# Kernel tuning notes

Measured on AMD Instinct MI355X. Metric: run time of the kernel, lower is better.

## Reference

```python
import jax, jax.numpy as jnp
import numpy as np

D = 256; NH = 8; HD = D // NH; K = 5; K2 = K * K; NLAYER = 2; DFF = 1024
EPS = 1e-5

def _kernel_grid():
    # (K2, 2) offsets in (x, y), spanning the full reference box
    lin = jnp.linspace(-0.5, 0.5, K, dtype=jnp.float32)
    gy, gx = jnp.meshgrid(lin, lin, indexing='ij')
    return jnp.stack([gx.reshape(-1), gy.reshape(-1)], axis=-1)

def _ref_windows(B, H, W):
    # mirrors TransIFFEncoder._create_ref_windows: (B, L, 7) = [x, y, 0.5, w, h, 0.5, 0]
    ry = (jnp.arange(H, dtype=jnp.float32) + 0.5) / H
    rx = (jnp.arange(W, dtype=jnp.float32) + 0.5) / W
    gy, gx = jnp.meshgrid(ry, rx, indexing='ij')
    xy = jnp.stack([gx.reshape(-1), gy.reshape(-1)], axis=-1)
    L = H * W
    wh = jnp.full((L, 2), 0.025, jnp.float32)
    half = jnp.full((L, 1), 0.5, jnp.float32)
    zero = jnp.zeros((L, 1), jnp.float32)
    box = jnp.concatenate([xy, half, wh, half, zero], axis=-1)
    return jnp.broadcast_to(box[None], (B, L, 7))

def _layer_norm(x, g, b):
    m = jnp.mean(x, -1, keepdims=True)
    v = jnp.mean((x - m) ** 2, -1, keepdims=True)
    return (x - m) * jax.lax.rsqrt(v + EPS) * g + b

def _box_attn(q, v, ref, H, W, Wv, bv, Wbox, bbox, Wattn, battn, Wo, bo):
    # Box3dAttention (BoxeR-style), with_rotation=False, nlevel=1
    B, L, _ = q.shape
    val = (v @ Wv + bv).reshape(B, L, NH, HD)                         # value projection
    aw = jax.nn.softmax((q @ Wattn + battn).reshape(B, L, NH, K2), -1)  # attn over K2 samples
    off = (q @ Wbox + bbox).reshape(B, L, NH, 4)                      # box offsets per head
    refb = ref[:, :, None, jnp.array([0, 1, 3, 4])]                   # (B,L,1,4) -> x,y,w,h
    boxes = refb + off / 8.0 * refb[..., jnp.array([2, 3, 2, 3])]
    pts = boxes[..., None, :2] + boxes[..., None, 2:] * _kernel_grid()  # (B,L,NH,K2,2) in [0,1]
    # deformable-attn bilinear sampling: pixel = loc*size - 0.5, zero outside bounds
    x = pts[..., 0] * W - 0.5
    y = pts[..., 1] * H - 0.5
    x0 = jnp.floor(x); y0 = jnp.floor(y)
    vt = val.transpose(0, 2, 1, 3)   # (B,NH,L,HD); spatial axis L == H*W
    awt = aw.transpose(0, 2, 1, 3)   # (B,NH,L,K2)
    out = jnp.zeros((B, NH, L, HD), q.dtype)
    for dx in (0, 1):
        for dy in (0, 1):
            xi = x0 + dx; yi = y0 + dy
            wgt = (1.0 - jnp.abs(x - xi)) * (1.0 - jnp.abs(y - yi))
            valid = (xi >= 0) & (xi < W) & (yi >= 0) & (yi < H)
            idx = (jnp.clip(yi, 0, H - 1) * W + jnp.clip(xi, 0, W - 1)).astype(jnp.int32)
            idxt = idx.transpose(0, 2, 1, 3).reshape(B, NH, L * K2)
            g = jnp.take_along_axis(vt, idxt[..., None], axis=2).reshape(B, NH, L, K2, HD)
            wc = awt * jnp.where(valid, wgt, 0.0).transpose(0, 2, 1, 3)
            out = out + jnp.einsum('bnlk,bnlkd->bnld', wc, g)
    out = out.transpose(0, 2, 1, 3).reshape(B, L, D)
    return out @ Wo + bo

def setup_inputs() -> dict:
    key = jax.random.key(0)
    ks = jax.random.split(key, 10)
    B, H, W = 1, 128, 128
    s = 0.02
    f = jnp.float32
    return {
        'src': jax.random.normal(ks[0], (B, D, H, W), f),
        'pos': jax.random.normal(ks[1], (B, D, H, W), f),
        'Wv': jax.random.normal(ks[2], (NLAYER, D, D), f) * s,
        'bv': jnp.zeros((NLAYER, D), f),
        'Wbox': jax.random.normal(ks[3], (NLAYER, D, NH * 4), f) * s,
        'bbox': jnp.zeros((NLAYER, NH * 4), f),
        'Wattn': jax.random.normal(ks[4], (NLAYER, D, NH * K2), f) * s,
        'battn': jnp.zeros((NLAYER, NH * K2), f),
        'Wo': jax.random.normal(ks[5], (NLAYER, D, D), f) * s,
        'bo': jnp.zeros((NLAYER, D), f),
        'W1': jax.random.normal(ks[6], (NLAYER, D, DFF), f) * s,
        'b1': jnp.zeros((NLAYER, DFF), f),
        'W2': jax.random.normal(ks[7], (NLAYER, DFF, D), f) * s,
        'b2': jnp.zeros((NLAYER, D), f),
        'ln1_g': jnp.ones((NLAYER, D), f), 'ln1_b': jnp.zeros((NLAYER, D), f),
        'ln2_g': jnp.ones((NLAYER, D), f), 'ln2_b': jnp.zeros((NLAYER, D), f),
    }

def reference(src, pos, Wv, bv, Wbox, bbox, Wattn, battn, Wo, bo,
              W1, b1, W2, b2, ln1_g, ln1_b, ln2_g, ln2_b):
    B, C, H, W = src.shape
    x = src.reshape(B, C, H * W).transpose(0, 2, 1)   # flatten_with_shape
    p = pos.reshape(B, C, H * W).transpose(0, 2, 1)
    ref = _ref_windows(B, H, W)
    for i in range(NLAYER):
        q = x + p                                      # with_pos_embed
        a = _box_attn(q, x, ref, H, W, Wv[i], bv[i], Wbox[i], bbox[i],
                      Wattn[i], battn[i], Wo[i], bo[i])
        x = _layer_norm(x + a, ln1_g[i], ln1_b[i])
        ff = jax.nn.relu(x @ W1[i] + b1[i]) @ W2[i] + b2[i]
        x = _layer_norm(x + ff, ln2_g[i], ln2_b[i])
    return x
```

## Files before the change

kernel.cpp:

```cpp
#include <hip/hip_runtime.h>
#include <cstdint>
#include <cstddef>

typedef unsigned short u16;
typedef unsigned int u32;

#define L_TOK 16384
#define DMODEL 256
#define NHEAD 8
#define HDIM 32

typedef __attribute__((ext_vector_type(8))) short bf16x8;
typedef __attribute__((ext_vector_type(4))) float f32x4;
typedef __attribute__((ext_vector_type(4))) unsigned short u16x4;

__device__ __forceinline__ float bf2f(u16 u) {
    union { unsigned int i; float f; } v; v.i = ((unsigned int)u) << 16; return v.f;
}
__device__ __forceinline__ u16 f2bf(float f) {
    union { unsigned int i; float f; } v; v.f = f;
    unsigned int i = v.i;
    unsigned int r = (i + 0x7FFFu + ((i >> 16) & 1u)) >> 16;
    return (u16)r;
}

__device__ __forceinline__ void gload16(const u16* g, u16* l) {
    __builtin_amdgcn_global_load_lds((const __attribute__((address_space(1))) u32*)g,
                                     (__attribute__((address_space(3))) u32*)l, 16, 0, 0);
}

__global__ __launch_bounds__(256) void fill_kernel(float* __restrict__ out, int n, float v) {
    int t = blockIdx.x * 256 + threadIdx.x;
    if (t < n) out[t] = v;
}

__global__ __launch_bounds__(256) void xpose_tiled(const float* __restrict__ in,
                                                   u16* __restrict__ out) {
    __shared__ float t[64][65];
    int d0 = blockIdx.x * 64, l0 = blockIdx.y * 64;
    int c = threadIdx.x & 63, r4 = threadIdx.x >> 6;
#pragma unroll
    for (int it = 0; it < 16; ++it) {
        int r = it * 4 + r4;
        t[r][c] = in[(size_t)(d0 + r) * L_TOK + l0 + c];
    }
    __syncthreads();
#pragma unroll
    for (int it = 0; it < 16; ++it) {
        int r = it * 4 + r4;
        out[(size_t)(l0 + r) * DMODEL + d0 + c] = f2bf(t[c][r]);
    }
}

__global__ __launch_bounds__(256) void addq_tiled(const u16* __restrict__ x,
                                                  const float* __restrict__ p,
                                                  u16* __restrict__ q) {
    __shared__ float t[64][65];
    int d0 = blockIdx.x * 64, l0 = blockIdx.y * 64;
    int c = threadIdx.x & 63, r4 = threadIdx.x >> 6;
#pragma unroll
    for (int it = 0; it < 16; ++it) {
        int r = it * 4 + r4;
        t[r][c] = p[(size_t)(d0 + r) * L_TOK + l0 + c];
    }
    __syncthreads();
#pragma unroll
    for (int it = 0; it < 16; ++it) {
        int r = it * 4 + r4;
        size_t idx = (size_t)(l0 + r) * DMODEL + d0 + c;
        q[idx] = f2bf(bf2f(x[idx]) + t[c][r]);
    }
}

__global__ __launch_bounds__(256) void prepack_all(const float* __restrict__ Wattn,
                                                   const float* __restrict__ Wbox,
                                                   const float* __restrict__ battn,
                                                   const float* __restrict__ bbox,
                                                   const float* __restrict__ Wv,
                                                   const float* __restrict__ Wo,
                                                   const float* __restrict__ W1,
                                                   const float* __restrict__ W2,
                                                   u16* __restrict__ wbuf) {
    const int PER_LAYER = 720896;
    int idx = blockIdx.x * 256 + threadIdx.x;
    if (idx >= 2 * PER_LAYER) return;
    int layer = idx / PER_LAYER;
    int r = idx - layer * PER_LAYER;
    u16* wb = wbuf + (size_t)layer * 1474560;
    float w; u16* hi; u16* lo; int pos;
    if (r < 65536) {
        int n = r >> 8, k = r & 255;
        const float* Wa = Wattn + (size_t)layer * 51200;
        const float* Wb = Wbox  + (size_t)layer * 8192;
        w = (n < 200) ? Wa[(size_t)k * 200 + n]
                      : (n < 232 ? Wb[(size_t)k * 32 + (n - 200)] : 0.f);
        hi = wb; lo = wb + 65536; pos = r;
        if (k == 0) {
            float* bias = (float*)(wb + 131072);
            bias[n] = (n < 200) ? battn[layer * 200 + n]
                                : (n < 232 ? bbox[layer * 32 + n - 200] : 0.f);
        }
    } else if (r < 131072) {
        int rr = r - 65536; int n = rr >> 8, k = rr & 255;
        w = Wv[(size_t)layer * 65536 + (size_t)k * 256 + n];
        hi = wb + 163840; lo = wb + 229376; pos = rr;
    } else if (r < 196608) {
        int rr = r - 131072; int n = rr >> 8, k = rr & 255;
        w = Wo[(size_t)layer * 65536 + (size_t)k * 256 + n];
        hi = wb + 294912; lo = wb + 360448; pos = rr;
    } else if (r < 458752) {
        int rr = r - 196608; int n = rr >> 8, k = rr & 255;
        w = W1[(size_t)layer * 262144 + (size_t)k * 1024 + n];
        hi = wb + 425984; lo = wb + 688128; pos = rr;
    } else {
        int rr = r - 458752; int n = rr >> 10, k = rr & 1023;
        w = W2[(size_t)layer * 262144 + (size_t)k * 256 + n];
        hi = wb + 950272; lo = wb + 1212416; pos = rr;
    }
    u16 h = f2bf(w);
    hi[pos] = h;
    lo[pos] = f2bf(w - bf2f(h));
}

#define BN 64
#define BK 64

template<int BMv>
__global__ __launch_bounds__(256) void gemm_dual(const u16* __restrict__ Aa,
                                                 const u16* __restrict__ Bha,
                                                 const u16* __restrict__ Bla,
                                                 const float* __restrict__ biasa,
                                                 u16* __restrict__ Ca,
                                                 const u16* __restrict__ Ab,
                                                 const u16* __restrict__ Bhb,
                                                 const u16* __restrict__ Blb,
                                                 const float* __restrict__ biasb,
                                                 u16* __restrict__ Cb,
                                                 int K, int ldC, int relu, int ysplit) {
    constexpr int ASZ = BMv * BK;
    constexpr int BSZ = BN * BK;
    constexpr int ACH = BMv / 32;
    constexpr int NI  = BMv / 32;
    __shared__ __align__(16) u16 lds[2][ASZ + 2 * BSZ];

    const int tid  = threadIdx.x;
    const int lane = tid & 63;
    const int wave = tid >> 6;
    const int wm = wave >> 1, wn = wave & 1;
    const int row = lane & 15, kch = lane >> 4;

    const int nx = gridDim.x;
    const int nwg = nx * gridDim.y;
    int id = blockIdx.y * nx + blockIdx.x;
    if ((nwg & 7) == 0) { int qq = nwg >> 3; id = (id & 7) * qq + (id >> 3); }
    int by = id / nx;
    const int n0 = (id % nx) * BN;

    const int sel = by >= ysplit;
    if (sel) by -= ysplit;
    const int m0 = by * BMv;
    const u16*  A    = sel ? Ab    : Aa;
    const u16*  Bhi  = sel ? Bhb   : Bha;
    const u16*  Blo  = sel ? Blb   : Bla;
    const float* bias = sel ? biasb : biasa;
    u16*        C    = sel ? Cb    : Ca;

    const int srow  = tid >> 3;
    const int sslot = (tid & 7) ^ (srow & 7);
    const u16* ga  = A   + (size_t)(m0 + srow) * K + sslot * 8;
    const u16* gbh = Bhi + (size_t)(n0 + srow) * K + sslot * 8;
    const u16* gbl = Blo + (size_t)(n0 + srow) * K + sslot * 8;

    f32x4 acc[NI][2] = {};
    const int nkt = K / BK;

    auto stage = [&](int kt, int buf) {
        u16* lb = &lds[buf][0];
        const int ko = kt * BK;
#pragma unroll
        for (int it = 0; it < ACH; ++it)
            gload16(ga + ko + (size_t)it * 32 * K, lb + tid * 8 + it * 2048);
#pragma unroll
        for (int it = 0; it < 2; ++it) {
            gload16(gbh + ko + (size_t)it * 32 * K, lb + ASZ + tid * 8 + it * 2048);
            gload16(gbl + ko + (size_t)it * 32 * K, lb + ASZ + BSZ + tid * 8 + it * 2048);
        }
    };

    stage(0, 0);
    __syncthreads();
    for (int t = 0; t < nkt; ++t) {
        const int cur = t & 1;
        if (t + 1 < nkt) stage(t + 1, cur ^ 1);

        const u16* lb = &lds[cur][0];
#pragma unroll
        for (int kk = 0; kk < 2; ++kk) {
            const int ks = kk * 4 + kch;
            bf16x8 af[NI];
#pragma unroll
            for (int i = 0; i < NI; ++i) {
                const int r = wm * (BMv / 2) + i * 16 + row;
                af[i] = *(const bf16x8*)(lb + r * BK + ((ks ^ (r & 7)) * 8));
            }
#pragma unroll
            for (int j = 0; j < 2; ++j) {
                const int rb = wn * 32 + j * 16 + row;
                bf16x8 bh = *(const bf16x8*)(lb + ASZ + rb * BK + ((ks ^ (rb & 7)) * 8));
                bf16x8 bl = *(const bf16x8*)(lb + ASZ + BSZ + rb * BK + ((ks ^ (rb & 7)) * 8));
#pragma unroll
                for (int i = 0; i < NI; ++i) {
                    acc[i][j] = __builtin_amdgcn_mfma_f32_16x16x32_bf16(af[i], bh, acc[i][j], 0, 0, 0);
                    acc[i][j] = __builtin_amdgcn_mfma_f32_16x16x32_bf16(af[i], bl, acc[i][j], 0, 0, 0);
                }
            }
        }
        __syncthreads();
    }

    const int cm0 = m0 + wm * (BMv / 2) + (lane >> 4) * 4;
    const int cn0 = n0 + wn * 32 + (lane & 15);
#pragma unroll
    for (int j = 0; j < 2; ++j) {
        int cn = cn0 + j * 16;
        float bv_ = bias[cn];
#pragma unroll
        for (int i = 0; i < NI; ++i) {
#pragma unroll
            for (int r = 0; r < 4; ++r) {
                float v = acc[i][j][r] + bv_;
                if (relu) v = fmaxf(v, 0.f);
                C[(size_t)(cm0 + i * 16 + r) * ldC + cn] = f2bf(v);
            }
        }
    }
}

__global__ __launch_bounds__(256) void softmax_kernel(u16* __restrict__ awb, int total) {
    int t = blockIdx.x * blockDim.x + threadIdx.x;
    if (t >= total) return;
    int l = t >> 3, n = t & 7;
    u16* pp = awb + (size_t)l * 256 + n * 25;
    float v[25];
    float mx = -1e30f;
    for (int k = 0; k < 25; k++) { v[k] = bf2f(pp[k]); mx = fmaxf(mx, v[k]); }
    float s = 0.f;
    for (int k = 0; k < 25; k++) { v[k] = __expf(v[k] - mx); s += v[k]; }
    float inv = 1.f / s;
    for (int k = 0; k < 25; k++) pp[k] = f2bf(v[k] * inv);
}

__global__ __launch_bounds__(256) void sample_kernel(const u16* __restrict__ val,
                                                     const u16* __restrict__ awb,
                                                     u16* __restrict__ out) {
    int tid = blockIdx.x * 256 + threadIdx.x;
    int ch = tid & 3;
    int pair = tid >> 2;
    int n = pair & 7;
    int l = pair >> 3;
    int iy = l >> 7, ix = l & 127;
    float cx = (ix + 0.5f) * (1.f / 128.f);
    float cy = (iy + 0.5f) * (1.f / 128.f);
    const u16* rowp = awb + (size_t)l * 256;
    const u16* o = rowp + 200 + n * 4;
    float bx = cx + bf2f(o[0]) * (0.025f / 8.f);
    float by = cy + bf2f(o[1]) * (0.025f / 8.f);
    float bw = 0.025f + bf2f(o[2]) * (0.025f / 8.f);
    float bh = 0.025f + bf2f(o[3]) * (0.025f / 8.f);
    const u16* awp = rowp + n * 25;
    const u16* vbase = val + n * 32 + ch * 8;
    float acc[8] = {};
    for (int k = 0; k < 25; k++) {
        float gx = (float)(k % 5 - 2) * 0.25f;
        float gy = (float)(k / 5 - 2) * 0.25f;
        float xx = (bx + bw * gx) * 128.f - 0.5f;
        float yy = (by + bh * gy) * 128.f - 0.5f;
        float x0 = floorf(xx), y0 = floorf(yy);
        float a_ = bf2f(awp[k]);
#pragma unroll
        for (int dy = 0; dy < 2; dy++) {
#pragma unroll
            for (int dx = 0; dx < 2; dx++) {
                float xi = x0 + dx, yi = y0 + dy;
                float w_ = (1.f - fabsf(xx - xi)) * (1.f - fabsf(yy - yi)) * a_;
                bool valid = (xi >= 0.f) & (xi < 128.f) & (yi >= 0.f) & (yi < 128.f);
                w_ = valid ? w_ : 0.f;
                int ixi = min(max((int)xi, 0), 127);
                int iyi = min(max((int)yi, 0), 127);
                int idx = iyi * 128 + ixi;
                bf16x8 v = *(const bf16x8*)(vbase + (size_t)idx * 256);
#pragma unroll
                for (int e = 0; e < 8; e++)
                    acc[e] += w_ * bf2f((u16)v[e]);
            }
        }
    }
    bf16x8 ov;
#pragma unroll
    for (int e = 0; e < 8; e++) ov[e] = (short)f2bf(acc[e]);
    *(bf16x8*)(out + (size_t)l * 256 + n * 32 + ch * 8) = ov;
}

__global__ __launch_bounds__(256) void ln_rows_bf16(const u16* __restrict__ xin,
                                                    const u16* __restrict__ delta,
                                                    const float* __restrict__ g,
                                                    const float* __restrict__ b,
                                                    u16* __restrict__ out) {
    int lane = threadIdx.x & 63;
    int row = blockIdx.x * 4 + (threadIdx.x >> 6);
    size_t base = (size_t)row * 256 + lane * 4;
    u16x4 xv = *(const u16x4*)(xin + base);
    u16x4 dv = *(const u16x4*)(delta + base);
    float v[4]; float s = 0.f, q = 0.f;
#pragma unroll
    for (int j = 0; j < 4; j++) {
        v[j] = bf2f(xv[j]) + bf2f(dv[j]);
        s += v[j]; q += v[j] * v[j];
    }
#pragma unroll
    for (int off = 1; off < 64; off <<= 1) {
        s += __shfl_xor(s, off, 64);
        q += __shfl_xor(q, off, 64);
    }
    float m = s * (1.f / 256.f);
    float var = q * (1.f / 256.f) - m * m;
    float r = rsqrtf(var + 1e-5f);
    f32x4 gv = *(const f32x4*)(g + lane * 4);
    f32x4 bv2 = *(const f32x4*)(b + lane * 4);
    u16x4 ov;
#pragma unroll
    for (int j = 0; j < 4; j++)
        ov[j] = f2bf((v[j] - m) * r * gv[j] + bv2[j]);
    *(u16x4*)(out + base) = ov;
}

__global__ __launch_bounds__(256) void ln_rows_f32(const u16* __restrict__ xin,
                                                   const u16* __restrict__ delta,
                                                   const float* __restrict__ g,
                                                   const float* __restrict__ b,
                                                   float* __restrict__ out) {
    int lane = threadIdx.x & 63;
    int row = blockIdx.x * 4 + (threadIdx.x >> 6);
    size_t base = (size_t)row * 256 + lane * 4;
    u16x4 xv = *(const u16x4*)(xin + base);
    u16x4 dv = *(const u16x4*)(delta + base);
    float v[4]; float s = 0.f, q = 0.f;
#pragma unroll
    for (int j = 0; j < 4; j++) {
        v[j] = bf2f(xv[j]) + bf2f(dv[j]);
        s += v[j]; q += v[j] * v[j];
    }
#pragma unroll
    for (int off = 1; off < 64; off <<= 1) {
        s += __shfl_xor(s, off, 64);
        q += __shfl_xor(q, off, 64);
    }
    float m = s * (1.f / 256.f);
    float var = q * (1.f / 256.f) - m * m;
    float r = rsqrtf(var + 1e-5f);
    f32x4 gv = *(const f32x4*)(g + lane * 4);
    f32x4 bv2 = *(const f32x4*)(b + lane * 4);
    f32x4 ov;
#pragma unroll
    for (int j = 0; j < 4; j++)
        ov[j] = (v[j] - m) * r * gv[j] + bv2[j];
    *(f32x4*)(out + base) = ov;
}

extern "C" void kernel_launch(void* const* d_in, const int* in_sizes, int n_in,
                              void* d_out, int out_size, void* d_ws, size_t ws_size,
                              hipStream_t stream) {
    const size_t MiB = 1048576;
    float* outp = (float*)d_out;
    int fillg = (out_size + 255) / 256;

    const int exp_sizes[18] = {4194304, 4194304, 131072, 512, 16384, 64, 102400, 400,
                               131072, 512, 524288, 2048, 524288, 512, 512, 512, 512, 512};
    bool env_ok = (n_in == 18) && (ws_size >= 25 * MiB) && (out_size == 4194304);
    if (env_ok) for (int i = 0; i < 18; i++) env_ok = env_ok && (in_sizes[i] == exp_sizes[i]);
    if (!env_ok) {
        hipLaunchKernelGGL(fill_kernel, dim3(fillg), dim3(256), 0, stream, outp, out_size, 3000.f);
        return;
    }

    const float* srcp  = (const float*)d_in[0];
    const float* posp  = (const float*)d_in[1];
    const float* Wv    = (const float*)d_in[2];
    const float* bv    = (const float*)d_in[3];
    const float* Wbox  = (const float*)d_in[4];
    const float* bbox  = (const float*)d_in[5];
    const float* Wattn = (const float*)d_in[6];
    const float* battn = (const float*)d_in[7];
    const float* Wo    = (const float*)d_in[8];
    const float* bo    = (const float*)d_in[9];
    const float* W1    = (const float*)d_in[10];
    const float* b1    = (const float*)d_in[11];
    const float* W2    = (const float*)d_in[12];
    const float* b2    = (const float*)d_in[13];
    const float* ln1g  = (const float*)d_in[14];
    const float* ln1b  = (const float*)d_in[15];
    const float* ln2g  = (const float*)d_in[16];
    const float* ln2b  = (const float*)d_in[17];

    char* ws = (char*)d_ws;
    u16* x       = (u16*)(ws + 0);
    u16* val     = (u16*)(ws + 8 * MiB);
    u16* hiddenA = (u16*)(ws + 8 * MiB);
    u16* awb     = (u16*)(ws + 16 * MiB);
    u16* tmp     = (u16*)(ws + 16 * MiB);
    u16* ffnout  = (u16*)(ws + 16 * MiB);
    u16* q       = (u16*)d_out;
    u16* attn    = (u16*)d_out;
    u16* hiddenB = (u16*)d_out;
    u16* wbuf    = (u16*)((char*)d_out + 8 * MiB);
    const size_t LSTR = 1474560;

    const int ND = L_TOK * DMODEL;
    const int BIG = 1 << 20;

    auto GD128 = [&](const u16* Aa, const u16* Bha, const u16* Bla, const float* ba_,
                     u16* Ca, const u16* Ab, const u16* Bhb, const u16* Blb,
                     const float* bb_, u16* Cb, int gx, int gy, int K, int ldC,
                     int relu, int ysplit) {
        hipLaunchKernelGGL((gemm_dual<128>), dim3(gx, gy), dim3(256), 0, stream,
                           Aa, Bha, Bla, ba_, Ca, Ab, Bhb, Blb, bb_, Cb, K, ldC, relu, ysplit);
    };
    auto GD64 = [&](const u16* Aa, const u16* Bha, const u16* Bla, const float* ba_,
                    u16* Ca, const u16* Ab, const u16* Bhb, const u16* Blb,
                    const float* bb_, u16* Cb, int gx, int gy, int K, int ldC,
                    int relu, int ysplit) {
        hipLaunchKernelGGL((gemm_dual<64>), dim3(gx, gy), dim3(256), 0, stream,
                           Aa, Bha, Bla, ba_, Ca, Ab, Bhb, Blb, bb_, Cb, K, ldC, relu, ysplit);
    };

    hipLaunchKernelGGL(prepack_all, dim3((2 * 720896 + 255) / 256), dim3(256), 0, stream,
                       Wattn, Wbox, battn, bbox, Wv, Wo, W1, W2, wbuf);

    hipLaunchKernelGGL(xpose_tiled, dim3(4, 256), dim3(256), 0, stream, srcp, x);

    for (int i = 0; i < 2; i++) {
        u16* wb = wbuf + (size_t)i * LSTR;

        hipLaunchKernelGGL(addq_tiled, dim3(4, 256), dim3(256), 0, stream, x, posp, q);

        GD128(q, wb + 0,      wb + 65536,  (const float*)(wb + 131072), awb,
              x, wb + 163840, wb + 229376, bv + (size_t)i * 256,       val,
              4, 256, 256, 256, 0, 128);

        hipLaunchKernelGGL(softmax_kernel, dim3((L_TOK * NHEAD + 255) / 256), dim3(256), 0,
                           stream, awb, L_TOK * NHEAD);

        hipLaunchKernelGGL(sample_kernel, dim3(L_TOK * NHEAD * 4 / 256), dim3(256), 0, stream,
                           val, awb, attn);

        GD128(attn, wb + 294912, wb + 360448, bo + (size_t)i * 256, tmp,
              attn, wb + 294912, wb + 360448, bo + (size_t)i * 256, tmp,
              4, 128, 256, 256, 0, BIG);

        hipLaunchKernelGGL(ln_rows_bf16, dim3(L_TOK / 4), dim3(256), 0, stream,
                           x, tmp, ln1g + (size_t)i * 256, ln1b + (size_t)i * 256, x);

        for (int c = 0; c < 2; c++) {
            const u16* xa = x + (size_t)c * 8192 * 256;
            u16* ya = ffnout + (size_t)c * 8192 * 256;
            GD128(xa,                         wb + 425984, wb + 688128, b1 + (size_t)i * 1024, hiddenA,
                  xa + (size_t)4096 * 256,    wb + 425984, wb + 688128, b1 + (size_t)i * 1024, hiddenB,
                  16, 64, 256, 1024, 1, 32);
            GD64(hiddenA, wb + 950272, wb + 1212416, b2 + (size_t)i * 256, ya,
                 hiddenB, wb + 950272, wb + 1212416, b2 + (size_t)i * 256, ya + (size_t)4096 * 256,
                 4, 128, 1024, 256, 0, 64);
        }

        if (i == 0) {
            hipLaunchKernelGGL(ln_rows_bf16, dim3(L_TOK / 4), dim3(256), 0, stream,
                               x, ffnout, ln2g, ln2b, x);
        } else {
            hipLaunchKernelGGL(ln_rows_f32, dim3(L_TOK / 4), dim3(256), 0, stream,
                               x, ffnout, ln2g + 256, ln2b + 256, outp);
        }
    }
}
```

Measured before the change: 420.5 us.

## Fuse softmax into sampling kernel and add interior fast path for bilinear taps

Removes the standalone softmax kernel and recomputes the per-head softmax over the 25 attention logits inside the sampling kernel, with each of the 4 channel-threads redoing the max and sum. This drops one launch and a read-modify-write pass over the attention buffer. It also adds a branch for boxes fully inside the feature map that skips the per-tap bounds checks and clamping and loads the four neighbours from a single base pointer. The cost is redundant exp work per thread, plus a slight change in numerics because the softmax weights are no longer rounded to bf16.

```diff
diff --git a/kernel.cpp b/kernel.cpp
--- a/kernel.cpp
+++ b/kernel.cpp
@@ -236,20 +236,6 @@
     }
 }
 
-__global__ __launch_bounds__(256) void softmax_kernel(u16* __restrict__ awb, int total) {
-    int t = blockIdx.x * blockDim.x + threadIdx.x;
-    if (t >= total) return;
-    int l = t >> 3, n = t & 7;
-    u16* pp = awb + (size_t)l * 256 + n * 25;
-    float v[25];
-    float mx = -1e30f;
-    for (int k = 0; k < 25; k++) { v[k] = bf2f(pp[k]); mx = fmaxf(mx, v[k]); }
-    float s = 0.f;
-    for (int k = 0; k < 25; k++) { v[k] = __expf(v[k] - mx); s += v[k]; }
-    float inv = 1.f / s;
-    for (int k = 0; k < 25; k++) pp[k] = f2bf(v[k] * inv);
-}
-
 __global__ __launch_bounds__(256) void sample_kernel(const u16* __restrict__ val,
                                                      const u16* __restrict__ awb,
                                                      u16* __restrict__ out) {
@@ -269,29 +255,70 @@
     float bh = 0.025f + bf2f(o[3]) * (0.025f / 8.f);
     const u16* awp = rowp + n * 25;
     const u16* vbase = val + n * 32 + ch * 8;
+
+    float mx = -1e30f;
+#pragma unroll 1
+    for (int k = 0; k < 25; k++) mx = fmaxf(mx, bf2f(awp[k]));
+    float s = 0.f;
+#pragma unroll 1
+    for (int k = 0; k < 25; k++) s += __expf(bf2f(awp[k]) - mx);
+    float inv = 1.f / s;
+
+    float bx128 = bx * 128.f - 0.5f;
+    float by128 = by * 128.f - 0.5f;
+    float bwq = bw * 32.f;
+    float bhq = bh * 32.f;
+    float ax = 2.f * fabsf(bwq), ay = 2.f * fabsf(bhq);
+    bool interior = (bx128 - ax >= 0.f) & (bx128 + ax < 127.f) &
+                    (by128 - ay >= 0.f) & (by128 + ay < 127.f);
+
     float acc[8] = {};
-    for (int k = 0; k < 25; k++) {
-        float gx = (float)(k % 5 - 2) * 0.25f;
-        float gy = (float)(k / 5 - 2) * 0.25f;
-        float xx = (bx + bw * gx) * 128.f - 0.5f;
-        float yy = (by + bh * gy) * 128.f - 0.5f;
-        float x0 = floorf(xx), y0 = floorf(yy);
-        float a_ = bf2f(awp[k]);
-#pragma unroll
-        for (int dy = 0; dy < 2; dy++) {
-#pragma unroll
-            for (int dx = 0; dx < 2; dx++) {
-                float xi = x0 + dx, yi = y0 + dy;
-                float w_ = (1.f - fabsf(xx - xi)) * (1.f - fabsf(yy - yi)) * a_;
-                bool valid = (xi >= 0.f) & (xi < 128.f) & (yi >= 0.f) & (yi < 128.f);
-                w_ = valid ? w_ : 0.f;
-                int ixi = min(max((int)xi, 0), 127);
-                int iyi = min(max((int)yi, 0), 127);
-                int idx = iyi * 128 + ixi;
-                bf16x8 v = *(const bf16x8*)(vbase + (size_t)idx * 256);
-#pragma unroll
-                for (int e = 0; e < 8; e++)
-                    acc[e] += w_ * bf2f((u16)v[e]);
+    if (interior) {
+#pragma unroll 1
+        for (int k = 0; k < 25; k++) {
+            float xx = bx128 + (float)(k % 5 - 2) * bwq;
+            float yy = by128 + (float)(k / 5 - 2) * bhq;
+            float x0 = floorf(xx), y0 = floorf(yy);
+            float fx = xx - x0, fy = yy - y0;
+            float a_ = __expf(bf2f(awp[k]) - mx) * inv;
+            float gx0 = 1.f - fx, gy0 = 1.f - fy;
+            float w00 = gx0 * gy0 * a_;
+            float w01 = fx * gy0 * a_;
+            float w10 = gx0 * fy * a_;
+            float w11 = fx * fy * a_;
+            const u16* p00 = vbase + ((size_t)((int)y0 * 128 + (int)x0)) * 256;
+            bf16x8 v00 = *(const bf16x8*)(p00);
+            bf16x8 v01 = *(const bf16x8*)(p00 + 256);
+            bf16x8 v10 = *(const bf16x8*)(p00 + 128 * 256);
+            bf16x8 v11 = *(const bf16x8*)(p00 + 128 * 256 + 256);
+#pragma unroll
+            for (int e = 0; e < 8; e++)
+                acc[e] += w00 * bf2f((u16)v00[e]) + w01 * bf2f((u16)v01[e]) +
+                          w10 * bf2f((u16)v10[e]) + w11 * bf2f((u16)v11[e]);
+        }
+    } else {
+#pragma unroll 1
+        for (int k = 0; k < 25; k++) {
+            float xx = bx128 + (float)(k % 5 - 2) * bwq;
+            float yy = by128 + (float)(k / 5 - 2) * bhq;
+            float x0 = floorf(xx), y0 = floorf(yy);
+            float a_ = __expf(bf2f(awp[k]) - mx) * inv;
+#pragma unroll
+            for (int dy = 0; dy < 2; dy++) {
+#pragma unroll
+                for (int dx = 0; dx < 2; dx++) {
+                    float xi = x0 + dx, yi = y0 + dy;
+                    float w_ = (1.f - fabsf(xx - xi)) * (1.f - fabsf(yy - yi)) * a_;
+                    bool valid = (xi >= 0.f) & (xi < 128.f) & (yi >= 0.f) & (yi < 128.f);
+                    w_ = valid ? w_ : 0.f;
+                    int ixi = min(max((int)xi, 0), 127);
+                    int iyi = min(max((int)yi, 0), 127);
+                    int idx = iyi * 128 + ixi;
+                    bf16x8 v = *(const bf16x8*)(vbase + (size_t)idx * 256);
+#pragma unroll
+                    for (int e = 0; e < 8; e++)
+                        acc[e] += w_ * bf2f((u16)v[e]);
+                }
             }
         }
     }
@@ -447,9 +474,6 @@
               x, wb + 163840, wb + 229376, bv + (size_t)i * 256,       val,
               4, 256, 256, 256, 0, 128);
 
-        hipLaunchKernelGGL(softmax_kernel, dim3((L_TOK * NHEAD + 255) / 256), dim3(256), 0,
-                           stream, awb, L_TOK * NHEAD);
-
         hipLaunchKernelGGL(sample_kernel, dim3(L_TOK * NHEAD * 4 / 256), dim3(256), 0, stream,
                            val, awb, attn);
 
@@ -463,8 +487,8 @@
         for (int c = 0; c < 2; c++) {
             const u16* xa = x + (size_t)c * 8192 * 256;
             u16* ya = ffnout + (size_t)c * 8192 * 256;
-            GD128(xa,                         wb + 425984, wb + 688128, b1 + (size_t)i * 1024, hiddenA,
-                  xa + (size_t)4096 * 256,    wb + 425984, wb + 688128, b1 + (size_t)i * 1024, hiddenB,
+            GD128(xa,                      wb + 425984, wb + 688128, b1 + (size_t)i * 1024, hiddenA,
+                  xa + (size_t)4096 * 256, wb + 425984, wb + 688128, b1 + (size_t)i * 1024, hiddenB,
                   16, 64, 256, 1024, 1, 32);
             GD64(hiddenA, wb + 950272, wb + 1212416, b2 + (size_t)i * 256, ya,
                  hiddenB, wb + 950272, wb + 1212416, b2 + (size_t)i * 256, ya + (size_t)4096 * 256,
```

New measurement: 440.1 us. 4.7% more time.
